# Kernel tuning notes

Hardware: AMD Instinct MI355X
Metric: run time of the kernel (lower is better)

The kernel has to match this reference:

```python
import jax, jax.numpy as jnp
import numpy as np

B, C, H, W = 16, 1024, 32, 32  # H*W must equal C (required by matmul(h, fg) in the source)
EPS = 1e-5
NEG_SLOPE = 0.01


def setup_inputs() -> dict:
    key = jax.random.key(0)
    ks = jax.random.split(key, 12)
    s = 1.0 / np.sqrt(C)
    inp = {"x": jax.random.normal(ks[0], (B, C, H, W), jnp.float32)}
    for i, name in enumerate(["f", "g", "h", "c"]):
        inp[f"W{name}"] = jax.random.normal(ks[1 + 2 * i], (C, C), jnp.float32) * s
        inp[f"b{name}"] = jax.random.normal(ks[2 + 2 * i], (C,), jnp.float32) * 0.01
    inp["gamma"] = jnp.ones((C,), jnp.float32)
    inp["beta"] = jnp.zeros((C,), jnp.float32)
    inp["rmean"] = jax.random.normal(ks[9], (C,), jnp.float32) * 0.01
    inp["rvar"] = jax.random.uniform(ks[10], (C,), jnp.float32, 0.5, 1.5)
    return inp


def reference(x, Wf, bf, Wg, bg, Wh, bh, Wc, bc, gamma, beta, rmean, rvar):
    b, c, h_, w_ = x.shape
    n = h_ * w_  # == c by construction
    xf = x.reshape(b, c, n)

    def proj(Wp, bp):  # 1x1 conv == per-pixel channel matmul
        return jnp.einsum('oc,bcn->bon', Wp, xf) + bp[None, :, None]

    f = proj(Wf, bf)              # (B, C, N)
    g = proj(Wg, bg)              # (B, C, N); transposed(1,2) handled in einsum
    hh = proj(Wh, bh)             # (B, C, N)
    scores = jnp.einsum('bcn,bdn->bcd', f, g)        # f @ g^T -> (B, C, C)
    attn = jax.nn.softmax(scores, axis=1)            # softmax over dim=1 (as in source)
    # dropout2d(p=0.5) is identity in eval mode
    hfg = jnp.einsum('bcn,bnd->bcd', hh, attn)       # matmul(h, fg), needs N == C
    hfg = hfg.reshape(b, c, h_, w_)
    y = jnp.einsum('oc,bchw->bohw', Wc, hfg) + bc[None, :, None, None]
    y = jnp.where(y >= 0, y, NEG_SLOPE * y)          # LeakyReLU
    inv = gamma / jnp.sqrt(rvar + EPS)               # BatchNorm (eval mode)
    y = (y - rmean[None, :, None, None]) * inv[None, :, None, None] + beta[None, :, None, None]
    return y + x
```

## Files before the change

kernel.cpp:

```cpp
#include <hip/hip_runtime.h>
#include <cstdint>
#include <cstddef>

using half8  = __attribute__((ext_vector_type(8))) _Float16;
using half4  = __attribute__((ext_vector_type(4))) _Float16;
using float4v = __attribute__((ext_vector_type(4))) float;

#define CD 1024
#define M2 (1024 * 1024)

#define GLD16(gp, lp)                                                          \
    __builtin_amdgcn_global_load_lds(                                          \
        (const __attribute__((address_space(1))) void*)(gp),                   \
        (__attribute__((address_space(3))) void*)(lp), 16, 0, 0)

__global__ void prep_weights(const float* __restrict__ Wf, const float* __restrict__ Wg,
                             const float* __restrict__ Wh, const float* __restrict__ Wc,
                             const float* __restrict__ bf, const float* __restrict__ bg,
                             const float* __restrict__ bh,
                             _Float16* __restrict__ Wfgh, _Float16* __restrict__ WcH,
                             float* __restrict__ bstack) {
    int idx = blockIdx.x * 256 + threadIdx.x;
    if (idx < 3 * M2) {
        const float* s = idx < M2 ? Wf : (idx < 2 * M2 ? Wg : Wh);
        int off = idx & (M2 - 1);
        Wfgh[idx] = (_Float16)s[off];
    } else if (idx < 4 * M2) {
        WcH[idx - 3 * M2] = (_Float16)Wc[idx - 3 * M2];
    } else if (idx < 4 * M2 + 3 * CD) {
        int j = idx - 4 * M2;
        const float* s = j < CD ? bf : (j < 2 * CD ? bg : bh);
        bstack[j] = s[j & (CD - 1)];
    }
}

__global__ void transpose_x(const float* __restrict__ x, _Float16* __restrict__ xT, int b0) {
    __shared__ float tile[32][33];
    int z = blockIdx.z;
    const float* xb = x + (size_t)(b0 + z) * M2;
    _Float16* xTb = xT + (size_t)z * M2;
    int n0 = blockIdx.x * 32, k0 = blockIdx.y * 32;
    int tx = threadIdx.x, ty = threadIdx.y;
#pragma unroll
    for (int i = 0; i < 4; i++)
        tile[ty + i * 8][tx] = xb[(size_t)(k0 + ty + i * 8) * CD + n0 + tx];
    __syncthreads();
#pragma unroll
    for (int i = 0; i < 4; i++)
        xTb[(size_t)(n0 + ty + i * 8) * CD + k0 + tx] = (_Float16)tile[tx][ty + i * 8];
}

__global__ __launch_bounds__(256) void gemv_bch(const float* __restrict__ Wc,
                                                const float* __restrict__ bh,
                                                float* __restrict__ bch) {
    int o = blockIdx.x * 4 + (threadIdx.x >> 6);
    int lane = threadIdx.x & 63;
    float s = 0.f;
    for (int c = lane; c < CD; c += 64) s += Wc[(size_t)o * CD + c] * bh[c];
#pragma unroll
    for (int off = 32; off > 0; off >>= 1) s += __shfl_xor(s, off);
    if (lane == 0) bch[o] = s;
}

__global__ __launch_bounds__(256) void gemm128k(const _Float16* __restrict__ A,
                                                const _Float16* __restrict__ B,
                                                float* __restrict__ P) {
    __shared__ __align__(16) _Float16 As[128][32];
    __shared__ __align__(16) _Float16 Bs[128][32];
    int row0 = blockIdx.y * 128, col0 = blockIdx.x * 128;
    int koff = blockIdx.z * 256;
    int tid = threadIdx.x, lane = tid & 63, wave = tid >> 6;
    int wr = wave >> 1, wc = wave & 1;
    const int srow = lane >> 2;
    const int scol = (lane & 3) * 8;
    const size_t gA0 = (size_t)(row0 + wave * 16 + srow) * 1024 + koff + scol;
    const size_t gA1 = gA0 + (size_t)64 * 1024;
    const size_t gB0 = (size_t)(col0 + wave * 16 + srow) * 1024 + koff + scol;
    const size_t gB1 = gB0 + (size_t)64 * 1024;
    _Float16* ldsA0 = &As[wave * 16][0];
    _Float16* ldsA1 = &As[64 + wave * 16][0];
    _Float16* ldsB0 = &Bs[wave * 16][0];
    _Float16* ldsB1 = &Bs[64 + wave * 16][0];
    float4v acc[4][4] = {};
    const int kq = (lane >> 4) * 8, rl = lane & 15;
    for (int kt = 0; kt < 256; kt += 32) {
        GLD16(A + gA0 + kt, ldsA0);
        GLD16(A + gA1 + kt, ldsA1);
        GLD16(B + gB0 + kt, ldsB0);
        GLD16(B + gB1 + kt, ldsB1);
        __syncthreads();
        half8 af[4], bfr[4];
#pragma unroll
        for (int m = 0; m < 4; m++) af[m] = *(const half8*)(&As[wr * 64 + m * 16 + rl][kq]);
#pragma unroll
        for (int n = 0; n < 4; n++) bfr[n] = *(const half8*)(&Bs[wc * 64 + n * 16 + rl][kq]);
#pragma unroll
        for (int m = 0; m < 4; m++)
#pragma unroll
            for (int n = 0; n < 4; n++)
                acc[m][n] = __builtin_amdgcn_mfma_f32_16x16x32_f16(af[m], bfr[n], acc[m][n], 0, 0, 0);
        __syncthreads();
    }
    float* Pz = P + (size_t)blockIdx.z * M2;
#pragma unroll
    for (int m = 0; m < 4; m++)
#pragma unroll
        for (int r = 0; r < 4; r++) {
            int row = row0 + wr * 64 + m * 16 + ((lane >> 4) << 2) + r;
#pragma unroll
            for (int n = 0; n < 4; n++) {
                int col = col0 + wc * 64 + n * 16 + (lane & 15);
                Pz[(size_t)row * 1024 + col] = acc[m][n][r];
            }
        }
}

__global__ __launch_bounds__(256) void reduce_wch(const float* __restrict__ P,
                                                  _Float16* __restrict__ Wch) {
    int i = (blockIdx.x * 256 + threadIdx.x) * 4;
    float4v s = *(const float4v*)(P + i);
#pragma unroll
    for (int z = 1; z < 4; z++) {
        float4v v = *(const float4v*)(P + (size_t)z * M2 + i);
        s[0] += v[0]; s[1] += v[1]; s[2] += v[2]; s[3] += v[3];
    }
    half4 o;
#pragma unroll
    for (int j = 0; j < 4; j++) o[j] = (_Float16)s[j];
    *(half4*)(Wch + i) = o;
}

__global__ __launch_bounds__(256) void softmax_col(const float* __restrict__ ST,
                                                   _Float16* __restrict__ attnT) {
    int d = blockIdx.x, z = blockIdx.y;
    const float* row = ST + ((size_t)z * CD + d) * CD;
    _Float16* orow = attnT + ((size_t)z * CD + d) * CD;
    int t = threadIdx.x;
    float4v v = *(const float4v*)(row + t * 4);
    float mx = fmaxf(fmaxf(v[0], v[1]), fmaxf(v[2], v[3]));
#pragma unroll
    for (int o = 32; o > 0; o >>= 1) mx = fmaxf(mx, __shfl_xor(mx, o));
    __shared__ float redm[4], reds[4];
    int wave = t >> 6, lane = t & 63;
    if (lane == 0) redm[wave] = mx;
    __syncthreads();
    mx = fmaxf(fmaxf(redm[0], redm[1]), fmaxf(redm[2], redm[3]));
    float e[4];
    float s = 0.f;
#pragma unroll
    for (int i = 0; i < 4; i++) {
        e[i] = __expf(v[i] - mx);
        s += e[i];
    }
#pragma unroll
    for (int o = 32; o > 0; o >>= 1) s += __shfl_xor(s, o);
    if (lane == 0) reds[wave] = s;
    __syncthreads();
    s = reds[0] + reds[1] + reds[2] + reds[3];
    float inv = 1.0f / s;
    half4 ov;
#pragma unroll
    for (int i = 0; i < 4; i++) ov[i] = (_Float16)(e[i] * inv);
    *(half4*)(orow + t * 4) = ov;
}

enum { EP_F16B = 0, EP_F32 = 1, EP_F16 = 2, EP_FIN = 3 };

#define STG_A(T, BUF)                                                          \
    GLD16(gA + (size_t)(T) * 64 + 0 * 8192, &As[BUF][wv * 32 + 0][0]);         \
    GLD16(gA + (size_t)(T) * 64 + 1 * 8192, &As[BUF][wv * 32 + 8][0]);         \
    GLD16(gA + (size_t)(T) * 64 + 2 * 8192, &As[BUF][wv * 32 + 16][0]);        \
    GLD16(gA + (size_t)(T) * 64 + 3 * 8192, &As[BUF][wv * 32 + 24][0]);
#define STG_B(T, BUF)                                                          \
    GLD16(gB + (size_t)(T) * 64 + 0 * 8192, &Bs[BUF][wv * 32 + 0][0]);         \
    GLD16(gB + (size_t)(T) * 64 + 1 * 8192, &Bs[BUF][wv * 32 + 8][0]);         \
    GLD16(gB + (size_t)(T) * 64 + 2 * 8192, &Bs[BUF][wv * 32 + 16][0]);        \
    GLD16(gB + (size_t)(T) * 64 + 3 * 8192, &Bs[BUF][wv * 32 + 24][0]);

#define READS(SET, BUF, COL)                                                   \
    _Pragma("unroll") for (int m = 0; m < 4; m++)                              \
        a##SET[m] = *(const half8*)&As[BUF][wr * 64 + m * 16 + rl][COL];       \
    _Pragma("unroll") for (int n = 0; n < 4; n++)                              \
        b##SET[n] = *(const half8*)&Bs[BUF][wc * 64 + n * 16 + rl][COL];

#define MFMA16(SET)                                                            \
    __builtin_amdgcn_s_setprio(1);                                             \
    _Pragma("unroll") for (int m = 0; m < 4; m++)                              \
        _Pragma("unroll") for (int n = 0; n < 4; n++)                          \
            acc[m][n] = __builtin_amdgcn_mfma_f32_16x16x32_f16(                \
                a##SET[m], b##SET[n], acc[m][n], 0, 0, 0);                     \
    __builtin_amdgcn_s_setprio(0);

#define TILE64(BUF, OBUF, DOSTAGE, STT)                                        \
    {                                                                          \
        asm volatile("s_waitcnt vmcnt(0)" ::: "memory");                       \
        __builtin_amdgcn_sched_barrier(0);                                     \
        __builtin_amdgcn_s_barrier();                                          \
        READS(0, BUF, c0)                                                      \
        if (DOSTAGE) { STG_A(STT, OBUF) }                                      \
        MFMA16(0)                                                              \
        READS(1, BUF, c1)                                                      \
        if (DOSTAGE) { STG_B(STT, OBUF) }                                      \
        MFMA16(1)                                                              \
    }

template <int EPI>
__global__ __launch_bounds__(256, 2) void gemm_nt(
    const _Float16* __restrict__ A, int64_t sA, const _Float16* __restrict__ B, int64_t sB,
    void* __restrict__ Cp, int64_t sC, const float* __restrict__ bias,
    const float* __restrict__ bc, const float* __restrict__ gamma,
    const float* __restrict__ beta, const float* __restrict__ rmean,
    const float* __restrict__ rvar, const float* __restrict__ xres) {
    __shared__ __align__(16) _Float16 As[2][128][64];
    __shared__ __align__(16) _Float16 Bs[2][128][64];
    int z = blockIdx.z;
    const _Float16* Ab = A + (size_t)z * sA;
    const _Float16* Bb = B + (size_t)z * sB;
    int row0 = blockIdx.y * 128, col0 = blockIdx.x * 128;
    int tid = threadIdx.x, lane = tid & 63, wv = tid >> 6;
    int wr = wv >> 1, wc = wv & 1;

    const _Float16* gA = Ab + (size_t)(row0 + wv * 32 + (lane >> 3)) * 1024 +
                         ((lane & 7) ^ (lane >> 3)) * 8;
    const _Float16* gB = Bb + (size_t)(col0 + wv * 32 + (lane >> 3)) * 1024 +
                         ((lane & 7) ^ (lane >> 3)) * 8;

    const int rl = lane & 15;
    const int q = lane >> 4;
    const int c0 = ((q) ^ (rl & 7)) * 8;
    const int c1 = ((q + 4) ^ (rl & 7)) * 8;

    float4v acc[4][4] = {};
    half8 a0[4], b0[4], a1[4], b1[4];

    STG_A(0, 0) STG_B(0, 0)

#pragma unroll 1
    for (int g = 0; g < 7; ++g) {
        int t = 2 * g;
        TILE64(0, 1, 1, t + 1)
        TILE64(1, 0, 1, t + 2)
    }
    TILE64(0, 1, 1, 15)
    TILE64(1, 0, 0, 0)

#pragma unroll
    for (int m = 0; m < 4; m++) {
#pragma unroll
        for (int r = 0; r < 4; r++) {
            int row = row0 + wr * 64 + m * 16 + ((lane >> 4) << 2) + r;
            float add0 = 0.f, mu = 0.f, invs = 1.f, bet = 0.f;
            if constexpr (EPI == EP_F16B) add0 = bias[row];
            if constexpr (EPI == EP_FIN) {
                add0 = bc[row];
                mu = rmean[row];
                invs = gamma[row] * rsqrtf(rvar[row] + 1e-5f);
                bet = beta[row];
            }
#pragma unroll
            for (int n = 0; n < 4; n++) {
                int col = col0 + wc * 64 + n * 16 + (lane & 15);
                float v = acc[m][n][r];
                if constexpr (EPI == EP_F16B) {
                    ((_Float16*)Cp)[(size_t)z * sC + (size_t)row * 1024 + col] = (_Float16)(v + add0);
                } else if constexpr (EPI == EP_F32) {
                    ((float*)Cp)[(size_t)z * sC + (size_t)row * 1024 + col] = v;
                } else if constexpr (EPI == EP_F16) {
                    ((_Float16*)Cp)[(size_t)z * sC + (size_t)row * 1024 + col] = (_Float16)v;
                } else {
                    v += add0;
                    v = v >= 0.f ? v : 0.01f * v;
                    v = (v - mu) * invs + bet;
                    v += xres[(size_t)z * M2 + (size_t)row * 1024 + col];
                    ((float*)Cp)[(size_t)z * sC + (size_t)row * 1024 + col] = v;
                }
            }
        }
    }
}

extern "C" void kernel_launch(void* const* d_in, const int* in_sizes, int n_in,
                              void* d_out, int out_size, void* d_ws, size_t ws_size,
                              hipStream_t stream) {
    const float* x = (const float*)d_in[0];
    const float* Wf = (const float*)d_in[1];
    const float* bf = (const float*)d_in[2];
    const float* Wg = (const float*)d_in[3];
    const float* bg = (const float*)d_in[4];
    const float* Wh = (const float*)d_in[5];
    const float* bh = (const float*)d_in[6];
    const float* Wc = (const float*)d_in[7];
    const float* bc = (const float*)d_in[8];
    const float* gamma = (const float*)d_in[9];
    const float* beta = (const float*)d_in[10];
    const float* rmean = (const float*)d_in[11];
    const float* rvar = (const float*)d_in[12];

    char* p = (char*)d_ws;
    _Float16* Wfgh = (_Float16*)p;
    p += (size_t)3 * M2 * 2;
    _Float16* WcH = (_Float16*)p;
    p += (size_t)M2 * 2;
    float* bstack = (float*)p;
    p += (size_t)3 * CD * 4;
    size_t fixed = (size_t)(p - (char*)d_ws);
    fixed = (fixed + 255) & ~(size_t)255;

    size_t perB = (size_t)2 * M2 + (size_t)6 * M2 + (size_t)4 * M2;
    int nb = 16;
    while (nb > 1 && fixed + (size_t)nb * perB > ws_size) nb >>= 1;

    char* q = (char*)d_ws + fixed;

    {
        int total = 4 * M2 + 3 * CD;
        prep_weights<<<dim3((total + 255) / 256), dim3(256), 0, stream>>>(
            Wf, Wg, Wh, Wc, bf, bg, bh, Wfgh, WcH, bstack);
    }
    {
        _Float16* WhT = (_Float16*)q;
        float* Pk = (float*)(q + (size_t)2 * M2);
        transpose_x<<<dim3(32, 32, 1), dim3(32, 8), 0, stream>>>(Wh, WhT, 0);
        gemv_bch<<<dim3(256), dim3(256), 0, stream>>>(Wc, bh, bstack + 2 * CD);
        gemm128k<<<dim3(8, 8, 4), dim3(256), 0, stream>>>(WcH, WhT, Pk);
        reduce_wch<<<dim3(M2 / 1024), dim3(256), 0, stream>>>(Pk, Wfgh + (size_t)2 * M2);
    }

    for (int b0 = 0; b0 < 16; b0 += nb) {
        _Float16* xT = (_Float16*)q;
        _Float16* FGH = (_Float16*)(q + (size_t)nb * 2 * M2);
        float* ST = (float*)(q + (size_t)nb * 8 * M2);
        _Float16* attnT = xT;

        transpose_x<<<dim3(32, 32, nb), dim3(32, 8), 0, stream>>>(x, xT, b0);
        gemm_nt<EP_F16B><<<dim3(8, 24, nb), dim3(256), 0, stream>>>(
            Wfgh, 0, xT, M2, FGH, (int64_t)3 * M2, bstack,
            nullptr, nullptr, nullptr, nullptr, nullptr, nullptr);
        gemm_nt<EP_F32><<<dim3(8, 8, nb), dim3(256), 0, stream>>>(
            FGH + M2, (int64_t)3 * M2, FGH, (int64_t)3 * M2, ST, M2,
            nullptr, nullptr, nullptr, nullptr, nullptr, nullptr, nullptr);
        softmax_col<<<dim3(1024, nb), dim3(256), 0, stream>>>(ST, attnT);
        gemm_nt<EP_FIN><<<dim3(8, 8, nb), dim3(256), 0, stream>>>(
            FGH + (size_t)2 * M2, (int64_t)3 * M2, attnT, M2,
            (float*)d_out + (size_t)b0 * M2, M2,
            nullptr, bc, gamma, beta, rmean, rvar, x + (size_t)b0 * M2);
    }
}
```

Measured before the change: 315.5 us.

## Enlarge GEMM tiles to 256x256 with 8 waves and XCD-aware block swizzle

The batched GEMM kernel moves from 128x128 tiles with 4 waves to 256x256 tiles with 8 waves (512 threads). Each wave now computes a 128x64 sub-tile with an 8x4 accumulator array, which raises arithmetic intensity per LDS read. The launch grid is flattened to 1D and remapped so that blocks landing on the same XCD get neighbouring tiles, to improve L2 reuse. In exchange, LDS use doubles to 128KB per block and register pressure rises sharply, which can limit occupancy or cause spills. The grid shrinks fourfold, so small batch chunks may leave CUs idle.

Result: faster. 268.4 us (-14.9%).

```diff
diff --git a/kernel.cpp b/kernel.cpp
--- a/kernel.cpp
+++ b/kernel.cpp
@@ -178,14 +178,14 @@
     GLD16(gB + (size_t)(T) * 64 + 3 * 8192, &Bs[BUF][wv * 32 + 24][0]);
 
 #define READS(SET, BUF, COL)                                                   \
-    _Pragma("unroll") for (int m = 0; m < 4; m++)                              \
-        a##SET[m] = *(const half8*)&As[BUF][wr * 64 + m * 16 + rl][COL];       \
+    _Pragma("unroll") for (int m = 0; m < 8; m++)                              \
+        a##SET[m] = *(const half8*)&As[BUF][wr * 128 + m * 16 + rl][COL];      \
     _Pragma("unroll") for (int n = 0; n < 4; n++)                              \
         b##SET[n] = *(const half8*)&Bs[BUF][wc * 64 + n * 16 + rl][COL];
 
-#define MFMA16(SET)                                                            \
+#define MFMA32(SET)                                                            \
     __builtin_amdgcn_s_setprio(1);                                             \
-    _Pragma("unroll") for (int m = 0; m < 4; m++)                              \
+    _Pragma("unroll") for (int m = 0; m < 8; m++)                              \
         _Pragma("unroll") for (int n = 0; n < 4; n++)                          \
             acc[m][n] = __builtin_amdgcn_mfma_f32_16x16x32_f16(                \
                 a##SET[m], b##SET[n], acc[m][n], 0, 0, 0);                     \
@@ -198,27 +198,35 @@
         __builtin_amdgcn_s_barrier();                                          \
         READS(0, BUF, c0)                                                      \
         if (DOSTAGE) { STG_A(STT, OBUF) }                                      \
-        MFMA16(0)                                                              \
+        MFMA32(0)                                                              \
         READS(1, BUF, c1)                                                      \
         if (DOSTAGE) { STG_B(STT, OBUF) }                                      \
-        MFMA16(1)                                                              \
+        MFMA32(1)                                                              \
     }
 
 template <int EPI>
-__global__ __launch_bounds__(256, 2) void gemm_nt(
+__global__ __launch_bounds__(512, 2) void gemm_nt(
     const _Float16* __restrict__ A, int64_t sA, const _Float16* __restrict__ B, int64_t sB,
-    void* __restrict__ Cp, int64_t sC, const float* __restrict__ bias,
+    void* __restrict__ Cp, int64_t sC, int gx, int gy, const float* __restrict__ bias,
     const float* __restrict__ bc, const float* __restrict__ gamma,
     const float* __restrict__ beta, const float* __restrict__ rmean,
     const float* __restrict__ rvar, const float* __restrict__ xres) {
-    __shared__ __align__(16) _Float16 As[2][128][64];
-    __shared__ __align__(16) _Float16 Bs[2][128][64];
-    int z = blockIdx.z;
+    __shared__ __align__(16) _Float16 As[2][256][64];
+    __shared__ __align__(16) _Float16 Bs[2][256][64];
+
+    int flat = blockIdx.x;
+    int cpx = gridDim.x >> 3;
+    int swz = (flat & 7) * cpx + (flat >> 3);
+    int bx = swz % gx;
+    int rem = swz / gx;
+    int by = rem % gy;
+    int z = rem / gy;
+
     const _Float16* Ab = A + (size_t)z * sA;
     const _Float16* Bb = B + (size_t)z * sB;
-    int row0 = blockIdx.y * 128, col0 = blockIdx.x * 128;
+    int row0 = by * 256, col0 = bx * 256;
     int tid = threadIdx.x, lane = tid & 63, wv = tid >> 6;
-    int wr = wv >> 1, wc = wv & 1;
+    int wr = wv >> 2, wc = wv & 3;
 
     const _Float16* gA = Ab + (size_t)(row0 + wv * 32 + (lane >> 3)) * 1024 +
                          ((lane & 7) ^ (lane >> 3)) * 8;
@@ -230,8 +238,8 @@
     const int c0 = ((q) ^ (rl & 7)) * 8;
     const int c1 = ((q + 4) ^ (rl & 7)) * 8;
 
-    float4v acc[4][4] = {};
-    half8 a0[4], b0[4], a1[4], b1[4];
+    float4v acc[8][4] = {};
+    half8 a0[8], b0[4], a1[8], b1[4];
 
     STG_A(0, 0) STG_B(0, 0)
 
@@ -245,10 +253,10 @@
     TILE64(1, 0, 0, 0)
 
 #pragma unroll
-    for (int m = 0; m < 4; m++) {
+    for (int m = 0; m < 8; m++) {
 #pragma unroll
         for (int r = 0; r < 4; r++) {
-            int row = row0 + wr * 64 + m * 16 + ((lane >> 4) << 2) + r;
+            int row = row0 + wr * 128 + m * 16 + ((lane >> 4) << 2) + r;
             float add0 = 0.f, mu = 0.f, invs = 1.f, bet = 0.f;
             if constexpr (EPI == EP_F16B) add0 = bias[row];
             if constexpr (EPI == EP_FIN) {
@@ -333,16 +341,16 @@
         _Float16* attnT = xT;
 
         transpose_x<<<dim3(32, 32, nb), dim3(32, 8), 0, stream>>>(x, xT, b0);
-        gemm_nt<EP_F16B><<<dim3(8, 24, nb), dim3(256), 0, stream>>>(
-            Wfgh, 0, xT, M2, FGH, (int64_t)3 * M2, bstack,
+        gemm_nt<EP_F16B><<<dim3(4 * 12 * nb), dim3(512), 0, stream>>>(
+            Wfgh, 0, xT, M2, FGH, (int64_t)3 * M2, 4, 12, bstack,
             nullptr, nullptr, nullptr, nullptr, nullptr, nullptr);
-        gemm_nt<EP_F32><<<dim3(8, 8, nb), dim3(256), 0, stream>>>(
-            FGH + M2, (int64_t)3 * M2, FGH, (int64_t)3 * M2, ST, M2,
+        gemm_nt<EP_F32><<<dim3(4 * 4 * nb), dim3(512), 0, stream>>>(
+            FGH + M2, (int64_t)3 * M2, FGH, (int64_t)3 * M2, ST, M2, 4, 4,
             nullptr, nullptr, nullptr, nullptr, nullptr, nullptr, nullptr);
         softmax_col<<<dim3(1024, nb), dim3(256), 0, stream>>>(ST, attnT);
-        gemm_nt<EP_FIN><<<dim3(8, 8, nb), dim3(256), 0, stream>>>(
+        gemm_nt<EP_FIN><<<dim3(4 * 4 * nb), dim3(512), 0, stream>>>(
             FGH + (size_t)2 * M2, (int64_t)3 * M2, attnT, M2,
-            (float*)d_out + (size_t)b0 * M2, M2,
+            (float*)d_out + (size_t)b0 * M2, M2, 4, 4,
             nullptr, bc, gamma, beta, rmean, rvar, x + (size_t)b0 * M2);
     }
 }
```
